# Kernel tuning notes

Hardware: AMD Instinct MI355X
Metric: run time of the kernel (lower is better)

Reference implementation:

```python
import jax, jax.numpy as jnp
import numpy as np

B, N, F, H = 4, 40, 128, 128  # batch, num_nodes, in_features, hidden_features


def setup_inputs() -> dict:
    key = jax.random.key(0)
    ks = jax.random.split(key, 8)
    s = 0.02
    lengths = jax.random.randint(ks[0], (B,), N // 2, N + 1)
    mask = jnp.arange(N)[None, :] < lengths[:, None]  # (B, N) bool padding mask
    return dict(
        x=jax.random.normal(ks[1], (B, N, N, N, F), jnp.float32),
        mask=mask,
        Wi1=jax.random.normal(ks[2], (F, F), jnp.float32) * s, bi1=jnp.zeros((F,), jnp.float32),
        Wi2=jax.random.normal(ks[3], (F, H), jnp.float32) * s, bi2=jnp.zeros((H,), jnp.float32),
        We=jax.random.normal(ks[4], (H, H), jnp.float32) * s,
        Wo1=jax.random.normal(ks[5], (2 * H, 2 * H), jnp.float32) * s, bo1=jnp.zeros((2 * H,), jnp.float32),
        Wo2=jax.random.normal(ks[6], (2 * H, 1), jnp.float32) * s, bo2=jnp.zeros((1,), jnp.float32),
    )


def reference(x, mask, Wi1, bi1, Wi2, bi2, We, Wo1, bo1, Wo2, bo2):
    b, n = x.shape[0], x.shape[1]
    # inner MLP: F -> H, applied per hyperedge (B, n, n, n, H)
    x_embed = jnp.maximum(x @ Wi1 + bi1, 0.0) @ Wi2 + bi2
    # hyperedge validity: all three nodes unpadded AND strict ordering i < j < k
    idx = jnp.arange(n)
    ijk = (idx[:, None, None] < idx[None, :, None]) & (idx[None, :, None] < idx[None, None, :])  # (n,n,n)
    hm = (mask[:, :, None, None] & mask[:, None, :, None] & mask[:, None, None, :]) & ijk[None]  # (B,n,n,n)
    xf = x_embed.reshape(b, n * n * n, H)  # (B, n^3, H)
    logits = jnp.where(hm.reshape(b, n * n * n, 1), xf, -jnp.inf)
    a_flat = jax.nn.softmax(logits, axis=1)  # softmax over all n^3 hyperedges, per channel
    x_inner = jnp.maximum(xf @ We, 0.0)  # (B, n^3, H)
    h = jnp.concatenate([a_flat * x_inner, xf], axis=-1)  # (B, n^3, 2H)
    out = jnp.maximum(h @ Wo1 + bo1, 0.0) @ Wo2 + bo2  # (B, n^3, 1)
    return out.reshape(b, n, n, n)
```

## Files before the change

### kernel.cpp

```cpp
#include <hip/hip_runtime.h>

#define Bn 4
#define Nn 40
#define NCUBE 64000
#define ROWS 64
#define BPB  1000
#define MAXV 16384
#define CBLK 160

typedef _Float16 f16;
typedef __attribute__((ext_vector_type(8))) _Float16 f16x8;
typedef __attribute__((ext_vector_type(4))) _Float16 f16x4;
typedef __attribute__((ext_vector_type(4))) float f32x4;

#define OFF_WI1 0
#define OFF_WI2 16384
#define OFF_WE  32768
#define OFF_WO1 49152
#define WB_HALFS 114688
#define WB_BYTES (WB_HALFS*2)
#define WBOFF_COMPACT (4096 + Bn*MAXV*4)
#define WBOFF_SMALL   2560

__device__ __forceinline__ int swz8(int row, int colg) {
    return row*256 + (((colg & ~7) | ((colg ^ row) & 7)) << 3);
}
__device__ __forceinline__ int swzofs(int row, int col) {
    return swz8(row, col >> 3) + (col & 7);
}

template<bool PRE>
__device__ __forceinline__ f16x8 load_bfrag(const f16* __restrict__ WF,
                                            const float* __restrict__ W,
                                            int N, int NT, int kt, int nt, int l) {
    if constexpr (PRE) {
        return *(const f16x8*)(WF + ((kt*NT + nt)*64 + l)*8);
    } else {
        const int col = 16*nt + (l & 15);
        const int k0  = 32*kt + 8*(l >> 4);
        f16x8 r;
        #pragma unroll
        for (int j = 0; j < 8; ++j) r[j] = (f16)W[(k0 + j)*N + col];
        return r;
    }
}

__global__ __launch_bounds__(256)
void prepcount_kernel(const float* __restrict__ Wi1, const float* __restrict__ Wi2,
                      const float* __restrict__ We,  const float* __restrict__ Wo1,
                      f16* __restrict__ WB, const unsigned char* __restrict__ mask,
                      int* __restrict__ cnt, int* __restrict__ vlist) {
    const int blk = blockIdx.x;
    if (blk < 56) {
        int id = blk*256 + threadIdx.x;
        const float* W; int NT, N; f16* WF; int fid;
        if (id < 2048)      { W = Wi1; NT = 8;  N = 128; WF = WB+OFF_WI1; fid = id; }
        else if (id < 4096) { W = Wi2; NT = 8;  N = 128; WF = WB+OFF_WI2; fid = id-2048; }
        else if (id < 6144) { W = We;  NT = 8;  N = 128; WF = WB+OFF_WE;  fid = id-4096; }
        else                { W = Wo1; NT = 16; N = 256; WF = WB+OFF_WO1; fid = id-6144; }
        int frag = fid >> 6, l = fid & 63;
        int nt = frag % NT, kt = frag / NT;
        int col = 16*nt + (l & 15), k0 = 32*kt + 8*(l >> 4);
        #pragma unroll
        for (int j = 0; j < 8; ++j) WF[frag*512 + l*8 + j] = (f16)W[(k0 + j)*N + col];
    } else {
        const int idx = (blk - 56)*256 + threadIdx.x;
        const int b = idx / NCUBE, e = idx % NCUBE;
        const int k = e % Nn, ij = e / Nn, j = ij % Nn, i = ij / Nn;
        const bool v = (i < j) && (j < k) &&
                       mask[b*Nn+i] && mask[b*Nn+j] && mask[b*Nn+k];
        const unsigned long long m = __ballot(v);
        const int lane = threadIdx.x & 63;
        const int c = __popcll(m);
        int base = 0;
        if (lane == 0 && c) base = atomicAdd(&cnt[b], c);
        base = __shfl(base, 0);
        if (v) vlist[b*MAXV + base + __popcll(m & ((1ull<<lane)-1ull))] = e;
    }
}

template<bool PRE, bool COMPACT>
__global__ __launch_bounds__(512, 4)
void sums_kernel(const float* __restrict__ x, const unsigned char* __restrict__ mask,
                 const float* __restrict__ Wi1, const float* __restrict__ bi1,
                 const float* __restrict__ Wi2, const float* __restrict__ bi2,
                 float* __restrict__ sums, const int* __restrict__ cnt,
                 const int* __restrict__ vlist, const f16* __restrict__ WB)
{
    const int tid = threadIdx.x;
    const int l = tid & 63, w = tid >> 6, lr = l & 15, lg = l >> 4;
    const int wr = w >> 2, wc = w & 3;
    int b, r0;
    if (COMPACT) { b = blockIdx.x / CBLK; r0 = (blockIdx.x % CBLK)*ROWS; if (r0 >= cnt[b]) return; }
    else         { b = blockIdx.x / BPB;  r0 = (blockIdx.x % BPB)*ROWS; }

    __shared__ __align__(16) f16 hb[ROWS*256];
    __shared__ int earr[ROWS];
    __shared__ unsigned char mlds[Nn];
    __shared__ int anyv;

    if (!COMPACT) { if (tid < Nn) mlds[tid] = mask[b*Nn + tid]; if (tid == 0) anyv = 0; }
    if (tid < ROWS) {
        if (COMPACT) { int r = r0 + tid; earr[tid] = (r < cnt[b]) ? vlist[b*MAXV + r] : -1; }
        else earr[tid] = r0 + tid;
    }
    __syncthreads();

    bool rv[2];
    if (!COMPACT) {
        bool any = false;
        #pragma unroll
        for (int mt = 0; mt < 2; ++mt) {
            int e = earr[32*wr + 16*mt + lr];
            int k = e % Nn, ij = e / Nn, j = ij % Nn, i = ij / Nn;
            rv[mt] = (i < j) && (j < k) && mlds[i] && mlds[j] && mlds[k];
            any |= rv[mt];
        }
        if (any) anyv = 1;
        __syncthreads();
        if (!anyv) return;
    } else {
        #pragma unroll
        for (int mt = 0; mt < 2; ++mt) rv[mt] = (earr[32*wr + 16*mt + lr] >= 0);
    }

    #pragma unroll
    for (int p = 0; p < 4; ++p) {
        const int row = p*16 + (tid >> 5);
        const int c0  = (tid & 31)*4;
        int e = earr[row]; if (e < 0) e = 0;
        const float4 xv = *(const float4*)&x[((long)(b*NCUBE + e))*128 + c0];
        f16x4 v; v[0]=(f16)xv.x; v[1]=(f16)xv.y; v[2]=(f16)xv.z; v[3]=(f16)xv.w;
        *(f16x4*)&hb[swzofs(row, 128 + c0)] = v;
    }
    __syncthreads();

    {
        f32x4 acc1[2][2];
        #pragma unroll
        for (int n = 0; n < 2; ++n) {
            const float4 bv = *(const float4*)(bi1 + 16*(2*wc + n) + 4*lg);
            #pragma unroll
            for (int mt = 0; mt < 2; ++mt) {
                acc1[mt][n][0]=bv.x; acc1[mt][n][1]=bv.y; acc1[mt][n][2]=bv.z; acc1[mt][n][3]=bv.w;
            }
        }
        #pragma unroll
        for (int kt = 0; kt < 4; ++kt) {
            f16x8 bf[2];
            #pragma unroll
            for (int n = 0; n < 2; ++n)
                bf[n] = load_bfrag<PRE>(WB+OFF_WI1, Wi1, 128, 8, kt, 2*wc+n, l);
            #pragma unroll
            for (int mt = 0; mt < 2; ++mt) {
                const f16x8 af = *(const f16x8*)&hb[swz8(32*wr + 16*mt + lr, 16 + 4*kt + lg)];
                #pragma unroll
                for (int n = 0; n < 2; ++n)
                    acc1[mt][n] = __builtin_amdgcn_mfma_f32_16x16x32_f16(bf[n], af, acc1[mt][n], 0, 0, 0);
            }
        }
        #pragma unroll
        for (int mt = 0; mt < 2; ++mt)
            #pragma unroll
            for (int n = 0; n < 2; ++n) {
                f16x4 v;
                #pragma unroll
                for (int r = 0; r < 4; ++r) v[r] = (f16)fmaxf(acc1[mt][n][r], 0.f);
                *(f16x4*)&hb[swzofs(32*wr + 16*mt + lr, 16*(2*wc + n) + 4*lg)] = v;
            }
    }
    __syncthreads();

    f32x4 acc2[2][2];
    {
        #pragma unroll
        for (int n = 0; n < 2; ++n) {
            const float4 bv = *(const float4*)(bi2 + 16*(2*wc + n) + 4*lg);
            #pragma unroll
            for (int mt = 0; mt < 2; ++mt) {
                acc2[mt][n][0]=bv.x; acc2[mt][n][1]=bv.y; acc2[mt][n][2]=bv.z; acc2[mt][n][3]=bv.w;
            }
        }
        #pragma unroll
        for (int kt = 0; kt < 4; ++kt) {
            f16x8 bf[2];
            #pragma unroll
            for (int n = 0; n < 2; ++n)
                bf[n] = load_bfrag<PRE>(WB+OFF_WI2, Wi2, 128, 8, kt, 2*wc+n, l);
            #pragma unroll
            for (int mt = 0; mt < 2; ++mt) {
                const f16x8 af = *(const f16x8*)&hb[swz8(32*wr + 16*mt + lr, 4*kt + lg)];
                #pragma unroll
                for (int n = 0; n < 2; ++n)
                    acc2[mt][n] = __builtin_amdgcn_mfma_f32_16x16x32_f16(bf[n], af, acc2[mt][n], 0, 0, 0);
            }
        }
    }

    float s[2][4] = {{0,0,0,0},{0,0,0,0}};
    #pragma unroll
    for (int mt = 0; mt < 2; ++mt)
        if (rv[mt])
            #pragma unroll
            for (int n = 0; n < 2; ++n)
                #pragma unroll
                for (int r = 0; r < 4; ++r) s[n][r] += __expf(acc2[mt][n][r]);
    #pragma unroll
    for (int n = 0; n < 2; ++n)
        #pragma unroll
        for (int r = 0; r < 4; ++r) {
            float v = s[n][r];
            v += __shfl_xor(v, 1); v += __shfl_xor(v, 2);
            v += __shfl_xor(v, 4); v += __shfl_xor(v, 8);
            if (lr == 0) atomicAdd(&sums[b*128 + 16*(2*wc + n) + 4*lg + r], v);
        }
}

template<bool PRE>
__global__ __launch_bounds__(512, 4)
void full_kernel(const float* __restrict__ x, const unsigned char* __restrict__ mask,
                 const float* __restrict__ Wi1, const float* __restrict__ bi1,
                 const float* __restrict__ Wi2, const float* __restrict__ bi2,
                 const float* __restrict__ We,
                 const float* __restrict__ Wo1, const float* __restrict__ bo1,
                 const float* __restrict__ Wo2, const float* __restrict__ bo2,
                 const float* __restrict__ sums, const f16* __restrict__ WB,
                 float* __restrict__ out)
{
    const int tid = threadIdx.x;
    const int l = tid & 63, w = tid >> 6, lr = l & 15, lg = l >> 4;
    const int wr = w >> 2, wc = w & 3;
    const int b = blockIdx.x / BPB;
    const int e0 = (blockIdx.x % BPB) * ROWS;

    __shared__ __align__(16) f16 hb[ROWS*256];
    __shared__ float red[8][32];
    __shared__ unsigned char mlds[Nn];

    if (tid < Nn) mlds[tid] = mask[b*Nn + tid];

    #pragma unroll
    for (int p = 0; p < 4; ++p) {
        const int row = p*16 + (tid >> 5);
        const int c0  = (tid & 31)*4;
        const float4 xv = *(const float4*)&x[((long)(b*NCUBE + e0 + row))*128 + c0];
        f16x4 v; v[0]=(f16)xv.x; v[1]=(f16)xv.y; v[2]=(f16)xv.z; v[3]=(f16)xv.w;
        *(f16x4*)&hb[swzofs(row, 128 + c0)] = v;
    }
    __syncthreads();

    bool valid[2];
    #pragma unroll
    for (int mt = 0; mt < 2; ++mt) {
        int e = e0 + 32*wr + 16*mt + lr;
        int k = e % Nn, ij = e / Nn, j = ij % Nn, i = ij / Nn;
        valid[mt] = (i < j) && (j < k) && mlds[i] && mlds[j] && mlds[k];
    }

    {
        f32x4 acc1[2][2];
        #pragma unroll
        for (int n = 0; n < 2; ++n) {
            const float4 bv = *(const float4*)(bi1 + 16*(2*wc + n) + 4*lg);
            #pragma unroll
            for (int mt = 0; mt < 2; ++mt) {
                acc1[mt][n][0]=bv.x; acc1[mt][n][1]=bv.y; acc1[mt][n][2]=bv.z; acc1[mt][n][3]=bv.w;
            }
        }
        #pragma unroll
        for (int kt = 0; kt < 4; ++kt) {
            f16x8 bf[2];
            #pragma unroll
            for (int n = 0; n < 2; ++n)
                bf[n] = load_bfrag<PRE>(WB+OFF_WI1, Wi1, 128, 8, kt, 2*wc+n, l);
            #pragma unroll
            for (int mt = 0; mt < 2; ++mt) {
                const f16x8 af = *(const f16x8*)&hb[swz8(32*wr + 16*mt + lr, 16 + 4*kt + lg)];
                #pragma unroll
                for (int n = 0; n < 2; ++n)
                    acc1[mt][n] = __builtin_amdgcn_mfma_f32_16x16x32_f16(bf[n], af, acc1[mt][n], 0, 0, 0);
            }
        }
        #pragma unroll
        for (int mt = 0; mt < 2; ++mt)
            #pragma unroll
            for (int n = 0; n < 2; ++n) {
                f16x4 v;
                #pragma unroll
                for (int r = 0; r < 4; ++r) v[r] = (f16)fmaxf(acc1[mt][n][r], 0.f);
                *(f16x4*)&hb[swzofs(32*wr + 16*mt + lr, 16*(2*wc + n) + 4*lg)] = v;
            }
    }
    __syncthreads();

    f32x4 acc2[2][2];
    {
        #pragma unroll
        for (int n = 0; n < 2; ++n) {
            const float4 bv = *(const float4*)(bi2 + 16*(2*wc + n) + 4*lg);
            #pragma unroll
            for (int mt = 0; mt < 2; ++mt) {
                acc2[mt][n][0]=bv.x; acc2[mt][n][1]=bv.y; acc2[mt][n][2]=bv.z; acc2[mt][n][3]=bv.w;
            }
        }
        #pragma unroll
        for (int kt = 0; kt < 4; ++kt) {
            f16x8 bf[2];
            #pragma unroll
            for (int n = 0; n < 2; ++n)
                bf[n] = load_bfrag<PRE>(WB+OFF_WI2, Wi2, 128, 8, kt, 2*wc+n, l);
            #pragma unroll
            for (int mt = 0; mt < 2; ++mt) {
                const f16x8 af = *(const f16x8*)&hb[swz8(32*wr + 16*mt + lr, 4*kt + lg)];
                #pragma unroll
                for (int n = 0; n < 2; ++n)
                    acc2[mt][n] = __builtin_amdgcn_mfma_f32_16x16x32_f16(bf[n], af, acc2[mt][n], 0, 0, 0);
            }
        }
        #pragma unroll
        for (int mt = 0; mt < 2; ++mt)
            #pragma unroll
            for (int n = 0; n < 2; ++n) {
                f16x4 v;
                #pragma unroll
                for (int r = 0; r < 4; ++r) v[r] = (f16)acc2[mt][n][r];
                *(f16x4*)&hb[swzofs(32*wr + 16*mt + lr, 128 + 16*(2*wc + n) + 4*lg)] = v;
            }
        #pragma unroll
        for (int n = 0; n < 2; ++n) {
            const float4 sv = *(const float4*)(sums + b*128 + 16*(2*wc + n) + 4*lg);
            const float rinv[4] = {1.f/sv.x, 1.f/sv.y, 1.f/sv.z, 1.f/sv.w};
            #pragma unroll
            for (int mt = 0; mt < 2; ++mt)
                #pragma unroll
                for (int r = 0; r < 4; ++r)
                    acc2[mt][n][r] = valid[mt] ? __expf(acc2[mt][n][r]) * rinv[r] : 0.0f;
        }
    }
    __syncthreads();

    {
        f32x4 acc3[2][2];
        #pragma unroll
        for (int mt = 0; mt < 2; ++mt)
            #pragma unroll
            for (int n = 0; n < 2; ++n) { acc3[mt][n][0]=0.f; acc3[mt][n][1]=0.f; acc3[mt][n][2]=0.f; acc3[mt][n][3]=0.f; }
        #pragma unroll
        for (int kt = 0; kt < 4; ++kt) {
            f16x8 ef[2];
            #pragma unroll
            for (int n = 0; n < 2; ++n)
                ef[n] = load_bfrag<PRE>(WB+OFF_WE, We, 128, 8, kt, 2*wc+n, l);
            #pragma unroll
            for (int mt = 0; mt < 2; ++mt) {
                const f16x8 af = *(const f16x8*)&hb[swz8(32*wr + 16*mt + lr, 16 + 4*kt + lg)];
                #pragma unroll
                for (int n = 0; n < 2; ++n)
                    acc3[mt][n] = __builtin_amdgcn_mfma_f32_16x16x32_f16(ef[n], af, acc3[mt][n], 0, 0, 0);
            }
        }
        #pragma unroll
        for (int mt = 0; mt < 2; ++mt)
            #pragma unroll
            for (int n = 0; n < 2; ++n) {
                f16x4 v;
                #pragma unroll
                for (int r = 0; r < 4; ++r)
                    v[r] = (f16)(acc2[mt][n][r] * fmaxf(acc3[mt][n][r], 0.f));
                *(f16x4*)&hb[swzofs(32*wr + 16*mt + lr, 16*(2*wc + n) + 4*lg)] = v;
            }
    }
    __syncthreads();

    f32x4 acc4[2][4];
    #pragma unroll
    for (int n = 0; n < 4; ++n) {
        const float4 bv = *(const float4*)(bo1 + 16*(4*wc + n) + 4*lg);
        #pragma unroll
        for (int mt = 0; mt < 2; ++mt) {
            acc4[mt][n][0]=bv.x; acc4[mt][n][1]=bv.y; acc4[mt][n][2]=bv.z; acc4[mt][n][3]=bv.w;
        }
    }
    #pragma unroll
    for (int kt = 0; kt < 8; ++kt) {
        f16x8 of[4];
        #pragma unroll
        for (int n = 0; n < 4; ++n)
            of[n] = load_bfrag<PRE>(WB+OFF_WO1, Wo1, 256, 16, kt, 4*wc+n, l);
        #pragma unroll
        for (int mt = 0; mt < 2; ++mt) {
            const f16x8 af = *(const f16x8*)&hb[swz8(32*wr + 16*mt + lr, 4*kt + lg)];
            #pragma unroll
            for (int n = 0; n < 4; ++n)
                acc4[mt][n] = __builtin_amdgcn_mfma_f32_16x16x32_f16(of[n], af, acc4[mt][n], 0, 0, 0);
        }
    }

    {
        float outp[2] = {0.f, 0.f};
        #pragma unroll
        for (int n = 0; n < 4; ++n) {
            const float4 wv = *(const float4*)(Wo2 + 16*(4*wc + n) + 4*lg);
            #pragma unroll
            for (int mt = 0; mt < 2; ++mt) {
                outp[mt] += fmaxf(acc4[mt][n][0], 0.f)*wv.x + fmaxf(acc4[mt][n][1], 0.f)*wv.y
                          + fmaxf(acc4[mt][n][2], 0.f)*wv.z + fmaxf(acc4[mt][n][3], 0.f)*wv.w;
            }
        }
        #pragma unroll
        for (int mt = 0; mt < 2; ++mt) {
            outp[mt] += __shfl_xor(outp[mt], 16);
            outp[mt] += __shfl_xor(outp[mt], 32);
        }
        if (l < 16) {
            #pragma unroll
            for (int mt = 0; mt < 2; ++mt) red[w][16*mt + lr] = outp[mt];
        }
        __syncthreads();
        if (tid < ROWS) {
            const int rg = (tid >> 5)*4, rr = tid & 31;
            out[(long)b*NCUBE + e0 + tid] =
                red[rg+0][rr] + red[rg+1][rr] + red[rg+2][rr] + red[rg+3][rr] + bo2[0];
        }
    }
}

extern "C" void kernel_launch(void* const* d_in, const int* in_sizes, int n_in,
                              void* d_out, int out_size, void* d_ws, size_t ws_size,
                              hipStream_t stream) {
    const float*         x    = (const float*)d_in[0];
    const unsigned char* mask = (const unsigned char*)d_in[1];
    const float* Wi1 = (const float*)d_in[2];
    const float* bi1 = (const float*)d_in[3];
    const float* Wi2 = (const float*)d_in[4];
    const float* bi2 = (const float*)d_in[5];
    const float* We  = (const float*)d_in[6];
    const float* Wo1 = (const float*)d_in[7];
    const float* bo1 = (const float*)d_in[8];
    const float* Wo2 = (const float*)d_in[9];
    const float* bo2 = (const float*)d_in[10];
    float* out  = (float*)d_out;
    float* sums = (float*)d_ws;
    int*   cnt   = (int*)((char*)d_ws + 2048);
    int*   vlist = (int*)((char*)d_ws + 4096);

    const bool compact = ws_size >= (size_t)(WBOFF_COMPACT + WB_BYTES);
    const size_t wboff = compact ? WBOFF_COMPACT : WBOFF_SMALL;
    const bool pre     = ws_size >= wboff + WB_BYTES;
    f16* WB = (f16*)((char*)d_ws + wboff);

    hipMemsetAsync(d_ws, 0, 2048 + Bn*sizeof(int), stream);

    if (compact) {
        prepcount_kernel<<<1056, 256, 0, stream>>>(Wi1, Wi2, We, Wo1, WB, mask, cnt, vlist);
        sums_kernel<true, true><<<Bn*CBLK, 512, 0, stream>>>(x, mask, Wi1, bi1, Wi2, bi2,
                                                             sums, cnt, vlist, WB);
        full_kernel<true><<<Bn*BPB, 512, 0, stream>>>(x, mask, Wi1, bi1, Wi2, bi2, We,
                                                      Wo1, bo1, Wo2, bo2, sums, WB, out);
    } else if (pre) {
        prepcount_kernel<<<56, 256, 0, stream>>>(Wi1, Wi2, We, Wo1, WB, mask, cnt, vlist);
        sums_kernel<true, false><<<Bn*BPB, 512, 0, stream>>>(x, mask, Wi1, bi1, Wi2, bi2,
                                                             sums, cnt, vlist, WB);
        full_kernel<true><<<Bn*BPB, 512, 0, stream>>>(x, mask, Wi1, bi1, Wi2, bi2, We,
                                                      Wo1, bo1, Wo2, bo2, sums, WB, out);
    } else {
        sums_kernel<false, false><<<Bn*BPB, 512, 0, stream>>>(x, mask, Wi1, bi1, Wi2, bi2,
                                                              sums, cnt, vlist, WB);
        full_kernel<false><<<Bn*BPB, 512, 0, stream>>>(x, mask, Wi1, bi1, Wi2, bi2, We,
                                                       Wo1, bo1, Wo2, bo2, sums, WB, out);
    }
}
```

Measured before the change: 266.6 us.

## Switch MLP matmuls to 32x32x16 MFMA and double full-kernel row tile

```diff
diff --git a/kernel.cpp b/kernel.cpp
--- a/kernel.cpp
+++ b/kernel.cpp
@@ -3,15 +3,18 @@
 #define Bn 4
 #define Nn 40
 #define NCUBE 64000
-#define ROWS 64
-#define BPB  1000
+#define ROWS 128
+#define BPB  500
+#define SROWS 64
+#define SBPB 1000
 #define MAXV 16384
 #define CBLK 160
 
 typedef _Float16 f16;
-typedef __attribute__((ext_vector_type(8))) _Float16 f16x8;
-typedef __attribute__((ext_vector_type(4))) _Float16 f16x4;
-typedef __attribute__((ext_vector_type(4))) float f32x4;
+typedef __attribute__((ext_vector_type(8)))  _Float16 f16x8;
+typedef __attribute__((ext_vector_type(4)))  _Float16 f16x4;
+typedef __attribute__((ext_vector_type(4)))  float    f32x4;
+typedef __attribute__((ext_vector_type(16))) float    f32x16;
 
 #define OFF_WI1 0
 #define OFF_WI2 16384
@@ -30,19 +33,23 @@
 }
 
 template<bool PRE>
-__device__ __forceinline__ f16x8 load_bfrag(const f16* __restrict__ WF,
+__device__ __forceinline__ f16x8 load_wfrag(const f16* __restrict__ WF,
                                             const float* __restrict__ W,
                                             int N, int NT, int kt, int nt, int l) {
     if constexpr (PRE) {
         return *(const f16x8*)(WF + ((kt*NT + nt)*64 + l)*8);
     } else {
-        const int col = 16*nt + (l & 15);
-        const int k0  = 32*kt + 8*(l >> 4);
+        const int col = nt*32 + (l & 31);
+        const int k0  = kt*16 + 8*(l >> 5);
         f16x8 r;
         #pragma unroll
         for (int j = 0; j < 8; ++j) r[j] = (f16)W[(k0 + j)*N + col];
         return r;
     }
+}
+
+__device__ __forceinline__ f16x8 lds_af(const f16* hb, int rowbase, int areag, int kt, int l) {
+    return *(const f16x8*)&hb[swz8(rowbase + (l & 31), areag + 2*kt + (l >> 5))];
 }
 
 __global__ __launch_bounds__(256)
@@ -54,13 +61,13 @@
     if (blk < 56) {
         int id = blk*256 + threadIdx.x;
         const float* W; int NT, N; f16* WF; int fid;
-        if (id < 2048)      { W = Wi1; NT = 8;  N = 128; WF = WB+OFF_WI1; fid = id; }
-        else if (id < 4096) { W = Wi2; NT = 8;  N = 128; WF = WB+OFF_WI2; fid = id-2048; }
-        else if (id < 6144) { W = We;  NT = 8;  N = 128; WF = WB+OFF_WE;  fid = id-4096; }
-        else                { W = Wo1; NT = 16; N = 256; WF = WB+OFF_WO1; fid = id-6144; }
+        if (id < 2048)      { W = Wi1; NT = 4; N = 128; WF = WB+OFF_WI1; fid = id; }
+        else if (id < 4096) { W = Wi2; NT = 4; N = 128; WF = WB+OFF_WI2; fid = id-2048; }
+        else if (id < 6144) { W = We;  NT = 4; N = 128; WF = WB+OFF_WE;  fid = id-4096; }
+        else                { W = Wo1; NT = 8; N = 256; WF = WB+OFF_WO1; fid = id-6144; }
         int frag = fid >> 6, l = fid & 63;
         int nt = frag % NT, kt = frag / NT;
-        int col = 16*nt + (l & 15), k0 = 32*kt + 8*(l >> 4);
+        int col = nt*32 + (l & 31), k0 = kt*16 + 8*(l >> 5);
         #pragma unroll
         for (int j = 0; j < 8; ++j) WF[frag*512 + l*8 + j] = (f16)W[(k0 + j)*N + col];
     } else {
@@ -88,132 +95,92 @@
                  const int* __restrict__ vlist, const f16* __restrict__ WB)
 {
     const int tid = threadIdx.x;
-    const int l = tid & 63, w = tid >> 6, lr = l & 15, lg = l >> 4;
+    const int l = tid & 63, w = tid >> 6, lr = l & 31, lh = l >> 5;
     const int wr = w >> 2, wc = w & 3;
     int b, r0;
-    if (COMPACT) { b = blockIdx.x / CBLK; r0 = (blockIdx.x % CBLK)*ROWS; if (r0 >= cnt[b]) return; }
-    else         { b = blockIdx.x / BPB;  r0 = (blockIdx.x % BPB)*ROWS; }
-
-    __shared__ __align__(16) f16 hb[ROWS*256];
-    __shared__ int earr[ROWS];
+    if (COMPACT) { b = blockIdx.x / CBLK; r0 = (blockIdx.x % CBLK)*SROWS; if (r0 >= cnt[b]) return; }
+    else         { b = blockIdx.x / SBPB; r0 = (blockIdx.x % SBPB)*SROWS; }
+
+    __shared__ __align__(16) f16 hb[SROWS*256];
+    __shared__ int earr[SROWS];
     __shared__ unsigned char mlds[Nn];
     __shared__ int anyv;
 
     if (!COMPACT) { if (tid < Nn) mlds[tid] = mask[b*Nn + tid]; if (tid == 0) anyv = 0; }
-    if (tid < ROWS) {
+    if (tid < SROWS) {
         if (COMPACT) { int r = r0 + tid; earr[tid] = (r < cnt[b]) ? vlist[b*MAXV + r] : -1; }
         else earr[tid] = r0 + tid;
     }
     __syncthreads();
 
-    bool rv[2];
-    if (!COMPACT) {
-        bool any = false;
-        #pragma unroll
-        for (int mt = 0; mt < 2; ++mt) {
-            int e = earr[32*wr + 16*mt + lr];
+    bool rv;
+    {
+        int e = earr[32*wr + lr];
+        if (!COMPACT) {
             int k = e % Nn, ij = e / Nn, j = ij % Nn, i = ij / Nn;
-            rv[mt] = (i < j) && (j < k) && mlds[i] && mlds[j] && mlds[k];
-            any |= rv[mt];
-        }
-        if (any) anyv = 1;
-        __syncthreads();
-        if (!anyv) return;
-    } else {
-        #pragma unroll
-        for (int mt = 0; mt < 2; ++mt) rv[mt] = (earr[32*wr + 16*mt + lr] >= 0);
-    }
-
-    #pragma unroll
-    for (int p = 0; p < 4; ++p) {
-        const int row = p*16 + (tid >> 5);
-        const int c0  = (tid & 31)*4;
+            rv = (i < j) && (j < k) && mlds[i] && mlds[j] && mlds[k];
+            if (__any(rv)) anyv = 1;
+            __syncthreads();
+            if (!anyv) return;
+        } else rv = (e >= 0);
+    }
+
+    #pragma unroll
+    for (int p = 0; p < 2; ++p) {
+        const int row = p*32 + (tid >> 4);
+        const int c0  = (tid & 15)*8;
         int e = earr[row]; if (e < 0) e = 0;
-        const float4 xv = *(const float4*)&x[((long)(b*NCUBE + e))*128 + c0];
-        f16x4 v; v[0]=(f16)xv.x; v[1]=(f16)xv.y; v[2]=(f16)xv.z; v[3]=(f16)xv.w;
-        *(f16x4*)&hb[swzofs(row, 128 + c0)] = v;
-    }
-    __syncthreads();
-
-    {
-        f32x4 acc1[2][2];
-        #pragma unroll
-        for (int n = 0; n < 2; ++n) {
-            const float4 bv = *(const float4*)(bi1 + 16*(2*wc + n) + 4*lg);
-            #pragma unroll
-            for (int mt = 0; mt < 2; ++mt) {
-                acc1[mt][n][0]=bv.x; acc1[mt][n][1]=bv.y; acc1[mt][n][2]=bv.z; acc1[mt][n][3]=bv.w;
-            }
-        }
-        #pragma unroll
-        for (int kt = 0; kt < 4; ++kt) {
-            f16x8 bf[2];
-            #pragma unroll
-            for (int n = 0; n < 2; ++n)
-                bf[n] = load_bfrag<PRE>(WB+OFF_WI1, Wi1, 128, 8, kt, 2*wc+n, l);
-            #pragma unroll
-            for (int mt = 0; mt < 2; ++mt) {
-                const f16x8 af = *(const f16x8*)&hb[swz8(32*wr + 16*mt + lr, 16 + 4*kt + lg)];
-                #pragma unroll
-                for (int n = 0; n < 2; ++n)
-                    acc1[mt][n] = __builtin_amdgcn_mfma_f32_16x16x32_f16(bf[n], af, acc1[mt][n], 0, 0, 0);
-            }
-        }
-        #pragma unroll
-        for (int mt = 0; mt < 2; ++mt)
-            #pragma unroll
-            for (int n = 0; n < 2; ++n) {
-                f16x4 v;
-                #pragma unroll
-                for (int r = 0; r < 4; ++r) v[r] = (f16)fmaxf(acc1[mt][n][r], 0.f);
-                *(f16x4*)&hb[swzofs(32*wr + 16*mt + lr, 16*(2*wc + n) + 4*lg)] = v;
-            }
-    }
-    __syncthreads();
-
-    f32x4 acc2[2][2];
-    {
-        #pragma unroll
-        for (int n = 0; n < 2; ++n) {
-            const float4 bv = *(const float4*)(bi2 + 16*(2*wc + n) + 4*lg);
-            #pragma unroll
-            for (int mt = 0; mt < 2; ++mt) {
-                acc2[mt][n][0]=bv.x; acc2[mt][n][1]=bv.y; acc2[mt][n][2]=bv.z; acc2[mt][n][3]=bv.w;
-            }
-        }
-        #pragma unroll
-        for (int kt = 0; kt < 4; ++kt) {
-            f16x8 bf[2];
-            #pragma unroll
-            for (int n = 0; n < 2; ++n)
-                bf[n] = load_bfrag<PRE>(WB+OFF_WI2, Wi2, 128, 8, kt, 2*wc+n, l);
-            #pragma unroll
-            for (int mt = 0; mt < 2; ++mt) {
-                const f16x8 af = *(const f16x8*)&hb[swz8(32*wr + 16*mt + lr, 4*kt + lg)];
-                #pragma unroll
-                for (int n = 0; n < 2; ++n)
-                    acc2[mt][n] = __builtin_amdgcn_mfma_f32_16x16x32_f16(bf[n], af, acc2[mt][n], 0, 0, 0);
-            }
-        }
-    }
-
-    float s[2][4] = {{0,0,0,0},{0,0,0,0}};
-    #pragma unroll
-    for (int mt = 0; mt < 2; ++mt)
-        if (rv[mt])
-            #pragma unroll
-            for (int n = 0; n < 2; ++n)
-                #pragma unroll
-                for (int r = 0; r < 4; ++r) s[n][r] += __expf(acc2[mt][n][r]);
-    #pragma unroll
-    for (int n = 0; n < 2; ++n)
-        #pragma unroll
-        for (int r = 0; r < 4; ++r) {
-            float v = s[n][r];
-            v += __shfl_xor(v, 1); v += __shfl_xor(v, 2);
-            v += __shfl_xor(v, 4); v += __shfl_xor(v, 8);
-            if (lr == 0) atomicAdd(&sums[b*128 + 16*(2*wc + n) + 4*lg + r], v);
-        }
+        const float4 x0 = *(const float4*)&x[((long)(b*NCUBE + e))*128 + c0];
+        const float4 x1 = *(const float4*)&x[((long)(b*NCUBE + e))*128 + c0 + 4];
+        f16x8 v; v[0]=(f16)x0.x; v[1]=(f16)x0.y; v[2]=(f16)x0.z; v[3]=(f16)x0.w;
+                 v[4]=(f16)x1.x; v[5]=(f16)x1.y; v[6]=(f16)x1.z; v[7]=(f16)x1.w;
+        *(f16x8*)&hb[swzofs(row, 128 + c0)] = v;
+    }
+    __syncthreads();
+
+    f32x16 acc;
+    #pragma unroll
+    for (int rg = 0; rg < 4; ++rg) {
+        const float4 bv = *(const float4*)(bi1 + 32*wc + 8*rg + 4*lh);
+        acc[rg*4+0]=bv.x; acc[rg*4+1]=bv.y; acc[rg*4+2]=bv.z; acc[rg*4+3]=bv.w;
+    }
+    #pragma unroll
+    for (int kt = 0; kt < 8; ++kt) {
+        const f16x8 wf = load_wfrag<PRE>(WB+OFF_WI1, Wi1, 128, 4, kt, wc, l);
+        const f16x8 af = lds_af(hb, 32*wr, 16, kt, l);
+        acc = __builtin_amdgcn_mfma_f32_32x32x16_f16(wf, af, acc, 0, 0, 0);
+    }
+    #pragma unroll
+    for (int rg = 0; rg < 4; ++rg) {
+        f16x4 v;
+        #pragma unroll
+        for (int q = 0; q < 4; ++q) v[q] = (f16)fmaxf(acc[rg*4+q], 0.f);
+        *(f16x4*)&hb[swzofs(32*wr + lr, 32*wc + 8*rg + 4*lh)] = v;
+    }
+    __syncthreads();
+
+    #pragma unroll
+    for (int rg = 0; rg < 4; ++rg) {
+        const float4 bv = *(const float4*)(bi2 + 32*wc + 8*rg + 4*lh);
+        acc[rg*4+0]=bv.x; acc[rg*4+1]=bv.y; acc[rg*4+2]=bv.z; acc[rg*4+3]=bv.w;
+    }
+    #pragma unroll
+    for (int kt = 0; kt < 8; ++kt) {
+        const f16x8 wf = load_wfrag<PRE>(WB+OFF_WI2, Wi2, 128, 4, kt, wc, l);
+        const f16x8 af = lds_af(hb, 32*wr, 0, kt, l);
+        acc = __builtin_amdgcn_mfma_f32_32x32x16_f16(wf, af, acc, 0, 0, 0);
+    }
+
+    float s[16];
+    #pragma unroll
+    for (int r = 0; r < 16; ++r) s[r] = rv ? __expf(acc[r]) : 0.0f;
+    #pragma unroll
+    for (int r = 0; r < 16; ++r) {
+        float v = s[r];
+        v += __shfl_xor(v, 1); v += __shfl_xor(v, 2);
+        v += __shfl_xor(v, 4); v += __shfl_xor(v, 8); v += __shfl_xor(v, 16);
+        if (lr == 0) atomicAdd(&sums[b*128 + 32*wc + 8*(r>>2) + 4*lh + (r&3)], v);
+    }
 }
 
 template<bool PRE>
@@ -228,199 +195,191 @@
                  float* __restrict__ out)
 {
     const int tid = threadIdx.x;
-    const int l = tid & 63, w = tid >> 6, lr = l & 15, lg = l >> 4;
+    const int l = tid & 63, w = tid >> 6, lr = l & 31, lh = l >> 5;
     const int wr = w >> 2, wc = w & 3;
     const int b = blockIdx.x / BPB;
     const int e0 = (blockIdx.x % BPB) * ROWS;
 
     __shared__ __align__(16) f16 hb[ROWS*256];
-    __shared__ float red[8][32];
+    __shared__ float red[8][64];
     __shared__ unsigned char mlds[Nn];
 
     if (tid < Nn) mlds[tid] = mask[b*Nn + tid];
 
     #pragma unroll
     for (int p = 0; p < 4; ++p) {
-        const int row = p*16 + (tid >> 5);
-        const int c0  = (tid & 31)*4;
-        const float4 xv = *(const float4*)&x[((long)(b*NCUBE + e0 + row))*128 + c0];
-        f16x4 v; v[0]=(f16)xv.x; v[1]=(f16)xv.y; v[2]=(f16)xv.z; v[3]=(f16)xv.w;
-        *(f16x4*)&hb[swzofs(row, 128 + c0)] = v;
+        const int row = p*32 + (tid >> 4);
+        const int c0  = (tid & 15)*8;
+        const long base = ((long)(b*NCUBE + e0 + row))*128 + c0;
+        const float4 x0 = *(const float4*)&x[base];
+        const float4 x1 = *(const float4*)&x[base + 4];
+        f16x8 v; v[0]=(f16)x0.x; v[1]=(f16)x0.y; v[2]=(f16)x0.z; v[3]=(f16)x0.w;
+                 v[4]=(f16)x1.x; v[5]=(f16)x1.y; v[6]=(f16)x1.z; v[7]=(f16)x1.w;
+        *(f16x8*)&hb[swzofs(row, 128 + c0)] = v;
     }
     __syncthreads();
 
     bool valid[2];
     #pragma unroll
     for (int mt = 0; mt < 2; ++mt) {
-        int e = e0 + 32*wr + 16*mt + lr;
+        int e = e0 + 64*wr + 32*mt + lr;
         int k = e % Nn, ij = e / Nn, j = ij % Nn, i = ij / Nn;
         valid[mt] = (i < j) && (j < k) && mlds[i] && mlds[j] && mlds[k];
     }
 
     {
-        f32x4 acc1[2][2];
-        #pragma unroll
-        for (int n = 0; n < 2; ++n) {
-            const float4 bv = *(const float4*)(bi1 + 16*(2*wc + n) + 4*lg);
-            #pragma unroll
-            for (int mt = 0; mt < 2; ++mt) {
-                acc1[mt][n][0]=bv.x; acc1[mt][n][1]=bv.y; acc1[mt][n][2]=bv.z; acc1[mt][n][3]=bv.w;
-            }
-        }
-        #pragma unroll
-        for (int kt = 0; kt < 4; ++kt) {
-            f16x8 bf[2];
-            #pragma unroll
-            for (int n = 0; n < 2; ++n)
-                bf[n] = load_bfrag<PRE>(WB+OFF_WI1, Wi1, 128, 8, kt, 2*wc+n, l);
-            #pragma unroll
-            for (int mt = 0; mt < 2; ++mt) {
-                const f16x8 af = *(const f16x8*)&hb[swz8(32*wr + 16*mt + lr, 16 + 4*kt + lg)];
-                #pragma unroll
-                for (int n = 0; n < 2; ++n)
-                    acc1[mt][n] = __builtin_amdgcn_mfma_f32_16x16x32_f16(bf[n], af, acc1[mt][n], 0, 0, 0);
+        f32x16 acc1[2];
+        #pragma unroll
+        for (int rg = 0; rg < 4; ++rg) {
+            const float4 bv = *(const float4*)(bi1 + 32*wc + 8*rg + 4*lh);
+            #pragma unroll
+            for (int mt = 0; mt < 2; ++mt) {
+                acc1[mt][rg*4+0]=bv.x; acc1[mt][rg*4+1]=bv.y;
+                acc1[mt][rg*4+2]=bv.z; acc1[mt][rg*4+3]=bv.w;
+            }
+        }
+        #pragma unroll
+        for (int kt = 0; kt < 8; ++kt) {
+            const f16x8 wf = load_wfrag<PRE>(WB+OFF_WI1, Wi1, 128, 4, kt, wc, l);
+            #pragma unroll
+            for (int mt = 0; mt < 2; ++mt) {
+                const f16x8 af = lds_af(hb, 64*wr + 32*mt, 16, kt, l);
+                acc1[mt] = __builtin_amdgcn_mfma_f32_32x32x16_f16(wf, af, acc1[mt], 0, 0, 0);
             }
         }
         #pragma unroll
         for (int mt = 0; mt < 2; ++mt)
             #pragma unroll
-            for (int n = 0; n < 2; ++n) {
+            for (int rg = 0; rg < 4; ++rg) {
                 f16x4 v;
                 #pragma unroll
-                for (int r = 0; r < 4; ++r) v[r] = (f16)fmaxf(acc1[mt][n][r], 0.f);
-                *(f16x4*)&hb[swzofs(32*wr + 16*mt + lr, 16*(2*wc + n) + 4*lg)] = v;
-            }
-    }
-    __syncthreads();
-
-    f32x4 acc2[2][2];
+                for (int q = 0; q < 4; ++q) v[q] = (f16)fmaxf(acc1[mt][rg*4+q], 0.f);
+                *(f16x4*)&hb[swzofs(64*wr + 32*mt + lr, 32*wc + 8*rg + 4*lh)] = v;
+            }
+    }
+    __syncthreads();
+
+    f32x16 acc2[2];
     {
         #pragma unroll
-        for (int n = 0; n < 2; ++n) {
-            const float4 bv = *(const float4*)(bi2 + 16*(2*wc + n) + 4*lg);
-            #pragma unroll
-            for (int mt = 0; mt < 2; ++mt) {
-                acc2[mt][n][0]=bv.x; acc2[mt][n][1]=bv.y; acc2[mt][n][2]=bv.z; acc2[mt][n][3]=bv.w;
-            }
-        }
-        #pragma unroll
-        for (int kt = 0; kt < 4; ++kt) {
-            f16x8 bf[2];
-            #pragma unroll
-            for (int n = 0; n < 2; ++n)
-                bf[n] = load_bfrag<PRE>(WB+OFF_WI2, Wi2, 128, 8, kt, 2*wc+n, l);
-            #pragma unroll
-            for (int mt = 0; mt < 2; ++mt) {
-                const f16x8 af = *(const f16x8*)&hb[swz8(32*wr + 16*mt + lr, 4*kt + lg)];
-                #pragma unroll
-                for (int n = 0; n < 2; ++n)
-                    acc2[mt][n] = __builtin_amdgcn_mfma_f32_16x16x32_f16(bf[n], af, acc2[mt][n], 0, 0, 0);
+        for (int rg = 0; rg < 4; ++rg) {
+            const float4 bv = *(const float4*)(bi2 + 32*wc + 8*rg + 4*lh);
+            #pragma unroll
+            for (int mt = 0; mt < 2; ++mt) {
+                acc2[mt][rg*4+0]=bv.x; acc2[mt][rg*4+1]=bv.y;
+                acc2[mt][rg*4+2]=bv.z; acc2[mt][rg*4+3]=bv.w;
+            }
+        }
+        #pragma unroll
+        for (int kt = 0; kt < 8; ++kt) {
+            const f16x8 wf = load_wfrag<PRE>(WB+OFF_WI2, Wi2, 128, 4, kt, wc, l);
+            #pragma unroll
+            for (int mt = 0; mt < 2; ++mt) {
+                const f16x8 af = lds_af(hb, 64*wr + 32*mt, 0, kt, l);
+                acc2[mt] = __builtin_amdgcn_mfma_f32_32x32x16_f16(wf, af, acc2[mt], 0, 0, 0);
             }
         }
         #pragma unroll
         for (int mt = 0; mt < 2; ++mt)
             #pragma unroll
-            for (int n = 0; n < 2; ++n) {
+            for (int rg = 0; rg < 4; ++rg) {
                 f16x4 v;
                 #pragma unroll
-                for (int r = 0; r < 4; ++r) v[r] = (f16)acc2[mt][n][r];
-                *(f16x4*)&hb[swzofs(32*wr + 16*mt + lr, 128 + 16*(2*wc + n) + 4*lg)] = v;
-            }
-        #pragma unroll
-        for (int n = 0; n < 2; ++n) {
-            const float4 sv = *(const float4*)(sums + b*128 + 16*(2*wc + n) + 4*lg);
+                for (int q = 0; q < 4; ++q) v[q] = (f16)acc2[mt][rg*4+q];
+                *(f16x4*)&hb[swzofs(64*wr + 32*mt + lr, 128 + 32*wc + 8*rg + 4*lh)] = v;
+            }
+        #pragma unroll
+        for (int rg = 0; rg < 4; ++rg) {
+            const float4 sv = *(const float4*)(sums + b*128 + 32*wc + 8*rg + 4*lh);
             const float rinv[4] = {1.f/sv.x, 1.f/sv.y, 1.f/sv.z, 1.f/sv.w};
             #pragma unroll
             for (int mt = 0; mt < 2; ++mt)
                 #pragma unroll
-                for (int r = 0; r < 4; ++r)
-                    acc2[mt][n][r] = valid[mt] ? __expf(acc2[mt][n][r]) * rinv[r] : 0.0f;
+                for (int q = 0; q < 4; ++q)
+                    acc2[mt][rg*4+q] = valid[mt] ? __expf(acc2[mt][rg*4+q]) * rinv[q] : 0.0f;
         }
     }
     __syncthreads();
 
     {
-        f32x4 acc3[2][2];
+        f32x16 acc3[2];
         #pragma unroll
         for (int mt = 0; mt < 2; ++mt)
             #pragma unroll
-            for (int n = 0; n < 2; ++n) { acc3[mt][n][0]=0.f; acc3[mt][n][1]=0.f; acc3[mt][n][2]=0.f; acc3[mt][n][3]=0.f; }
-        #pragma unroll
-        for (int kt = 0; kt < 4; ++kt) {
-            f16x8 ef[2];
-            #pragma unroll
-            for (int n = 0; n < 2; ++n)
-                ef[n] = load_bfrag<PRE>(WB+OFF_WE, We, 128, 8, kt, 2*wc+n, l);
-            #pragma unroll
-            for (int mt = 0; mt < 2; ++mt) {
-                const f16x8 af = *(const f16x8*)&hb[swz8(32*wr + 16*mt + lr, 16 + 4*kt + lg)];
-                #pragma unroll
-                for (int n = 0; n < 2; ++n)
-                    acc3[mt][n] = __builtin_amdgcn_mfma_f32_16x16x32_f16(ef[n], af, acc3[mt][n], 0, 0, 0);
+            for (int r = 0; r < 16; ++r) acc3[mt][r] = 0.f;
+        #pragma unroll
+        for (int kt = 0; kt < 8; ++kt) {
+            const f16x8 wf = load_wfrag<PRE>(WB+OFF_WE, We, 128, 4, kt, wc, l);
+            #pragma unroll
+            for (int mt = 0; mt < 2; ++mt) {
+                const f16x8 af = lds_af(hb, 64*wr + 32*mt, 16, kt, l);
+                acc3[mt] = __builtin_amdgcn_mfma_f32_32x32x16_f16(wf, af, acc3[mt], 0, 0, 0);
             }
         }
         #pragma unroll
         for (int mt = 0; mt < 2; ++mt)
             #pragma unroll
-            for (int n = 0; n < 2; ++n) {
+            for (int rg = 0; rg < 4; ++rg) {
                 f16x4 v;
                 #pragma unroll
-                for (int r = 0; r < 4; ++r)
-                    v[r] = (f16)(acc2[mt][n][r] * fmaxf(acc3[mt][n][r], 0.f));
-                *(f16x4*)&hb[swzofs(32*wr + 16*mt + lr, 16*(2*wc + n) + 4*lg)] = v;
-            }
-    }
-    __syncthreads();
-
-    f32x4 acc4[2][4];
-    #pragma unroll
-    for (int n = 0; n < 4; ++n) {
-        const float4 bv = *(const float4*)(bo1 + 16*(4*wc + n) + 4*lg);
+                for (int q = 0; q < 4; ++q)
+                    v[q] = (f16)(acc2[mt][rg*4+q] * fmaxf(acc3[mt][rg*4+q], 0.f));
+                *(f16x4*)&hb[swzofs(64*wr + 32*mt + lr, 32*wc + 8*rg + 4*lh)] = v;
+            }
+    }
+    __syncthreads();
+
+    f32x16 acc4[2][2];
+    #pragma unroll
+    for (int ntl = 0; ntl < 2; ++ntl)
+        #pragma unroll
+        for (int rg = 0; rg < 4; ++rg) {
+            const float4 bv = *(const float4*)(bo1 + 64*wc + 32*ntl + 8*rg + 4*lh);
+            #pragma unroll
+            for (int mt = 0; mt < 2; ++mt) {
+                acc4[mt][ntl][rg*4+0]=bv.x; acc4[mt][ntl][rg*4+1]=bv.y;
+                acc4[mt][ntl][rg*4+2]=bv.z; acc4[mt][ntl][rg*4+3]=bv.w;
+            }
+        }
+    #pragma unroll
+    for (int kt = 0; kt < 16; ++kt) {
+        f16x8 of0 = load_wfrag<PRE>(WB+OFF_WO1, Wo1, 256, 8, kt, 2*wc+0, l);
+        f16x8 of1 = load_wfrag<PRE>(WB+OFF_WO1, Wo1, 256, 8, kt, 2*wc+1, l);
         #pragma unroll
         for (int mt = 0; mt < 2; ++mt) {
-            acc4[mt][n][0]=bv.x; acc4[mt][n][1]=bv.y; acc4[mt][n][2]=bv.z; acc4[mt][n][3]=bv.w;
-        }
-    }
-    #pragma unroll
-    for (int kt = 0; kt < 8; ++kt) {
-        f16x8 of[4];
-        #pragma unroll
-        for (int n = 0; n < 4; ++n)
-            of[n] = load_bfrag<PRE>(WB+OFF_WO1, Wo1, 256, 16, kt, 4*wc+n, l);
-        #pragma unroll
-        for (int mt = 0; mt < 2; ++mt) {
-            const f16x8 af = *(const f16x8*)&hb[swz8(32*wr + 16*mt + lr, 4*kt + lg)];
-            #pragma unroll
-            for (int n = 0; n < 4; ++n)
-                acc4[mt][n] = __builtin_amdgcn_mfma_f32_16x16x32_f16(of[n], af, acc4[mt][n], 0, 0, 0);
+            const f16x8 af = lds_af(hb, 64*wr + 32*mt, 0, kt, l);
+            acc4[mt][0] = __builtin_amdgcn_mfma_f32_32x32x16_f16(of0, af, acc4[mt][0], 0, 0, 0);
+            acc4[mt][1] = __builtin_amdgcn_mfma_f32_32x32x16_f16(of1, af, acc4[mt][1], 0, 0, 0);
         }
     }
 
     {
         float outp[2] = {0.f, 0.f};
         #pragma unroll
-        for (int n = 0; n < 4; ++n) {
-            const float4 wv = *(const float4*)(Wo2 + 16*(4*wc + n) + 4*lg);
-            #pragma unroll
-            for (int mt = 0; mt < 2; ++mt) {
-                outp[mt] += fmaxf(acc4[mt][n][0], 0.f)*wv.x + fmaxf(acc4[mt][n][1], 0.f)*wv.y
-                          + fmaxf(acc4[mt][n][2], 0.f)*wv.z + fmaxf(acc4[mt][n][3], 0.f)*wv.w;
-            }
-        }
-        #pragma unroll
-        for (int mt = 0; mt < 2; ++mt) {
-            outp[mt] += __shfl_xor(outp[mt], 16);
-            outp[mt] += __shfl_xor(outp[mt], 32);
-        }
-        if (l < 16) {
-            #pragma unroll
-            for (int mt = 0; mt < 2; ++mt) red[w][16*mt + lr] = outp[mt];
+        for (int ntl = 0; ntl < 2; ++ntl)
+            #pragma unroll
+            for (int rg = 0; rg < 4; ++rg) {
+                const float4 wv = *(const float4*)(Wo2 + 64*wc + 32*ntl + 8*rg + 4*lh);
+                #pragma unroll
+                for (int mt = 0; mt < 2; ++mt) {
+                    outp[mt] += fmaxf(acc4[mt][ntl][rg*4+0], 0.f)*wv.x
+                              + fmaxf(acc4[mt][ntl][rg*4+1], 0.f)*wv.y
+                              + fmaxf(acc4[mt][ntl][rg*4+2], 0.f)*wv.z
+                              + fmaxf(acc4[mt][ntl][rg*4+3], 0.f)*wv.w;
+                }
+            }
+        #pragma unroll
+        for (int mt = 0; mt < 2; ++mt) outp[mt] += __shfl_xor(outp[mt], 32);
+        if (l < 32) {
+            red[w][lr]      = outp[0];
+            red[w][32 + lr] = outp[1];
         }
         __syncthreads();
         if (tid < ROWS) {
-            const int rg = (tid >> 5)*4, rr = tid & 31;
+            const int wr2 = tid >> 6, idx = tid & 63;
             out[(long)b*NCUBE + e0 + tid] =
-                red[rg+0][rr] + red[rg+1][rr] + red[rg+2][rr] + red[rg+3][rr] + bo2[0];
+                red[wr2*4+0][idx] + red[wr2*4+1][idx] +
+                red[wr2*4+2][idx] + red[wr2*4+3][idx] + bo2[0];
         }
     }
 }
@@ -459,13 +418,13 @@
                                                       Wo1, bo1, Wo2, bo2, sums, WB, out);
     } else if (pre) {
         prepcount_kernel<<<56, 256, 0, stream>>>(Wi1, Wi2, We, Wo1, WB, mask, cnt, vlist);
-        sums_kernel<true, false><<<Bn*BPB, 512, 0, stream>>>(x, mask, Wi1, bi1, Wi2, bi2,
-                                                             sums, cnt, vlist, WB);
+        sums_kernel<true, false><<<Bn*SBPB, 512, 0, stream>>>(x, mask, Wi1, bi1, Wi2, bi2,
+                                                              sums, cnt, vlist, WB);
         full_kernel<true><<<Bn*BPB, 512, 0, stream>>>(x, mask, Wi1, bi1, Wi2, bi2, We,
                                                       Wo1, bo1, Wo2, bo2, sums, WB, out);
     } else {
-        sums_kernel<false, false><<<Bn*BPB, 512, 0, stream>>>(x, mask, Wi1, bi1, Wi2, bi2,
-                                                              sums, cnt, vlist, WB);
+        sums_kernel<false, false><<<Bn*SBPB, 512, 0, stream>>>(x, mask, Wi1, bi1, Wi2, bi2,
+                                                               sums, cnt, vlist, WB);
         full_kernel<false><<<Bn*BPB, 512, 0, stream>>>(x, mask, Wi1, bi1, Wi2, bi2, We,
                                                        Wo1, bo1, Wo2, bo2, sums, WB, out);
     }
```

Result: no change. 271.1 us (+1.7%).
